# Kernel tuning notes

Hardware: AMD Instinct MI355X
Metric: run time of the kernel (lower is better)

## Reference

```python
import jax, jax.numpy as jnp
import numpy as np

N_NODES = 100000
N_EDGES = 3200000
N_FEAT = 512
HIDDEN = 16
N_CLASSES = 40


def gcn_conv(x, src, dst, W, b, num_nodes):
    # GCNConv with self-loops and symmetric normalization (default PyG settings).
    loop = jnp.arange(num_nodes)
    s = jnp.concatenate([src, loop])
    d = jnp.concatenate([dst, loop])
    deg = jax.ops.segment_sum(jnp.ones_like(s, dtype=x.dtype), d, num_segments=num_nodes)
    dinv = jnp.where(deg > 0, jax.lax.rsqrt(deg), 0.0)
    norm = dinv[s] * dinv[d]  # [E+N]
    h = x @ W  # [N, out]
    msg = h[s] * norm[:, None]  # gather + scale
    out = jax.ops.segment_sum(msg, d, num_segments=num_nodes)  # scatter-add
    return out + b


def setup_inputs() -> dict:
    key = jax.random.key(0)
    k1, k2, k3, k4 = jax.random.split(key, 4)
    x = jax.random.normal(k1, (N_NODES, N_FEAT), dtype=jnp.float32)
    edge_index = jax.random.randint(k2, (2, N_EDGES), 0, N_NODES, dtype=jnp.int64)
    W1 = jax.random.normal(k3, (N_FEAT, HIDDEN), dtype=jnp.float32) * 0.05
    b1 = jnp.zeros((HIDDEN,), dtype=jnp.float32)
    W2 = jax.random.normal(k4, (HIDDEN, N_CLASSES), dtype=jnp.float32) * 0.05
    b2 = jnp.zeros((N_CLASSES,), dtype=jnp.float32)
    return {"x": x, "edge_index": edge_index, "W1": W1, "b1": b1, "W2": W2, "b2": b2}


def reference(x, edge_index, W1, b1, W2, b2):
    num_nodes = x.shape[0]
    src, dst = edge_index[0], edge_index[1]
    h = gcn_conv(x, src, dst, W1, b1, num_nodes)
    h = jax.nn.relu(h)
    # dropout is identity in eval mode (training=False)
    out = gcn_conv(h, src, dst, W2, b2, num_nodes)
    return jax.nn.log_softmax(out, axis=1)
```

## Files before the change

### kernel.cpp

```cpp
#include <hip/hip_runtime.h>

#define N_NODES 100000
#define N_EDGES 3200000
#define N_FEAT 512
#define HIDDEN 16
#define N_CLASSES 40

#define SCAN_BLOCKS 98

#define CH    12800
#define NCH   8
#define NS    32
#define SLICE (N_EDGES / NS)
#define SL4   (SLICE / 4)

typedef int v4i __attribute__((ext_vector_type(4)));

__global__ __launch_bounds__(512) void k_p1(const int* __restrict__ dst,
                                            int* __restrict__ partS) {
    __shared__ int hist[CH];
    int tid = threadIdx.x;
    int s = blockIdx.x >> 3, j = blockIdx.x & 7;
    int base = j * CH;
    int lim = N_NODES - base; if (lim > CH) lim = CH;
    for (int i = tid; i < CH; i += 512) hist[i] = 0;
    __syncthreads();
    const v4i* dp = reinterpret_cast<const v4i*>(dst + s * SLICE);
    for (int i = tid; i < SL4; i += 512) {
        v4i d4 = __builtin_nontemporal_load(dp + i);
        unsigned a = (unsigned)(d4.x - base); if (a < (unsigned)lim) atomicAdd(&hist[a], 1);
        unsigned b = (unsigned)(d4.y - base); if (b < (unsigned)lim) atomicAdd(&hist[b], 1);
        unsigned c = (unsigned)(d4.z - base); if (c < (unsigned)lim) atomicAdd(&hist[c], 1);
        unsigned d = (unsigned)(d4.w - base); if (d < (unsigned)lim) atomicAdd(&hist[d], 1);
    }
    __syncthreads();
    for (int i = tid; i < lim; i += 512)
        partS[s * N_NODES + base + i] = hist[i];
}

__global__ __launch_bounds__(256) void k_colscan(int* __restrict__ partS,
                                                 int* __restrict__ deg,
                                                 float* __restrict__ dinv) {
    int n = blockIdx.x * 256 + threadIdx.x;
    if (n >= N_NODES) return;
    int run = 0;
    #pragma unroll
    for (int s = 0; s < NS; s++) {
        int idx = s * N_NODES + n;
        int v = partS[idx];
        partS[idx] = run;
        run += v;
    }
    deg[n] = run;
    dinv[n] = rsqrtf((float)(run + 1));
}


__global__ __launch_bounds__(1024) void k_scan_a(const int* __restrict__ cnt,
                                                 int* __restrict__ bsum) {
    int tid = threadIdx.x;
    int i = blockIdx.x * 1024 + tid;
    int v = (i < N_NODES) ? cnt[i] : 0;
    #pragma unroll
    for (int off = 32; off >= 1; off >>= 1) v += __shfl_xor(v, off, 64);
    __shared__ int ws[16];
    if ((tid & 63) == 0) ws[tid >> 6] = v;
    __syncthreads();
    if (tid == 0) {
        int s = 0;
        #pragma unroll
        for (int w = 0; w < 16; w++) s += ws[w];
        bsum[blockIdx.x] = s;
    }
}

__global__ __launch_bounds__(128) void k_scan_b(const int* __restrict__ bsum,
                                                int* __restrict__ boff) {
    int tid = threadIdx.x;
    int lane = tid & 63, wv = tid >> 6;
    int v = (tid < SCAN_BLOCKS) ? bsum[tid] : 0;
    int sc = v;
    #pragma unroll
    for (int off = 1; off < 64; off <<= 1) {
        int t = __shfl_up(sc, off, 64);
        if (lane >= off) sc += t;
    }
    __shared__ int wsum[2];
    if (lane == 63) wsum[wv] = sc;
    __syncthreads();
    int pre = (wv == 1) ? wsum[0] : 0;
    if (tid < SCAN_BLOCKS) boff[tid] = pre + sc - v;
}

__global__ __launch_bounds__(1024) void k_scan_c(const int* __restrict__ cnt,
                                                 const int* __restrict__ boff,
                                                 int* __restrict__ row_start) {
    int tid = threadIdx.x;
    int i = blockIdx.x * 1024 + tid;
    int lane = tid & 63, wv = tid >> 6;
    int v = (i < N_NODES) ? cnt[i] : 0;
    int sc = v;
    #pragma unroll
    for (int off = 1; off < 64; off <<= 1) {
        int t = __shfl_up(sc, off, 64);
        if (lane >= off) sc += t;
    }
    __shared__ int wsum[16];
    if (lane == 63) wsum[wv] = sc;
    __syncthreads();
    int pre = 0;
    #pragma unroll
    for (int w = 0; w < 16; w++) pre += (w < wv) ? wsum[w] : 0;
    int excl = boff[blockIdx.x] + pre + sc - v;
    if (i < N_NODES) row_start[i] = excl;
    if (i == N_NODES) row_start[N_NODES] = N_EDGES;
}

__global__ __launch_bounds__(512) void k_p2(const int* __restrict__ src,
                                            const int* __restrict__ dst,
                                            const int* __restrict__ partS,
                                            const int* __restrict__ row_start,
                                            const float* __restrict__ dinv,
                                            int2* __restrict__ edge_data) {
    __shared__ int cur[CH];
    int tid = threadIdx.x;
    int s = blockIdx.x >> 3, j = blockIdx.x & 7;
    int base = j * CH;
    int lim = N_NODES - base; if (lim > CH) lim = CH;
    for (int i = tid; i < lim; i += 512)
        cur[i] = row_start[base + i] + partS[s * N_NODES + base + i];
    __syncthreads();
    const v4i* dp = reinterpret_cast<const v4i*>(dst + s * SLICE);
    const v4i* sp = reinterpret_cast<const v4i*>(src + s * SLICE);
    for (int i = tid; i < SL4; i += 512) {
        v4i d4 = __builtin_nontemporal_load(dp + i);
        v4i s4 = __builtin_nontemporal_load(sp + i);
        {
            unsigned nl = (unsigned)(d4.x - base);
            if (nl < (unsigned)lim) {
                int slot = atomicAdd(&cur[nl], 1);
                edge_data[slot] = make_int2(s4.x, __float_as_int(dinv[s4.x] * dinv[d4.x]));
            }
        }
        {
            unsigned nl = (unsigned)(d4.y - base);
            if (nl < (unsigned)lim) {
                int slot = atomicAdd(&cur[nl], 1);
                edge_data[slot] = make_int2(s4.y, __float_as_int(dinv[s4.y] * dinv[d4.y]));
            }
        }
        {
            unsigned nl = (unsigned)(d4.z - base);
            if (nl < (unsigned)lim) {
                int slot = atomicAdd(&cur[nl], 1);
                edge_data[slot] = make_int2(s4.z, __float_as_int(dinv[s4.z] * dinv[d4.z]));
            }
        }
        {
            unsigned nl = (unsigned)(d4.w - base);
            if (nl < (unsigned)lim) {
                int slot = atomicAdd(&cur[nl], 1);
                edge_data[slot] = make_int2(s4.w, __float_as_int(dinv[s4.w] * dinv[d4.w]));
            }
        }
    }
}


#define KC 32
#define LDSW 36

__global__ __launch_bounds__(256) void k_gemm1(const float* __restrict__ x,
                                               const float* __restrict__ W1,
                                               float* __restrict__ h1) {
    __shared__ float xs[256 * LDSW];
    int tid = threadIdx.x;
    int row = blockIdx.x * 256 + tid;

    float acc[HIDDEN];
    #pragma unroll
    for (int j = 0; j < HIDDEN; j++) acc[j] = 0.f;

    int s_sub = tid >> 3;
    int s_k4  = tid & 7;

    for (int kc = 0; kc < N_FEAT; kc += KC) {
        __syncthreads();
        #pragma unroll
        for (int l = 0; l < 8; l++) {
            int srow = s_sub + l * 32;
            int grow = blockIdx.x * 256 + srow;
            int gr = grow < N_NODES ? grow : N_NODES - 1;
            float4 v = *reinterpret_cast<const float4*>(
                x + (size_t)gr * N_FEAT + kc + s_k4 * 4);
            *reinterpret_cast<float4*>(&xs[srow * LDSW + s_k4 * 4]) = v;
        }
        __syncthreads();

        const float* Wc = W1 + kc * HIDDEN;
        #pragma unroll
        for (int k4 = 0; k4 < 8; k4++) {
            float4 xv = *reinterpret_cast<const float4*>(&xs[tid * LDSW + k4 * 4]);
            const float* w0 = Wc + (k4 * 4 + 0) * HIDDEN;
            const float* w1 = Wc + (k4 * 4 + 1) * HIDDEN;
            const float* w2 = Wc + (k4 * 4 + 2) * HIDDEN;
            const float* w3 = Wc + (k4 * 4 + 3) * HIDDEN;
            #pragma unroll
            for (int j = 0; j < HIDDEN; j++) {
                acc[j] += xv.x * w0[j];
                acc[j] += xv.y * w1[j];
                acc[j] += xv.z * w2[j];
                acc[j] += xv.w * w3[j];
            }
        }
    }

    if (row < N_NODES) {
        float4* op = reinterpret_cast<float4*>(h1 + (size_t)row * HIDDEN);
        #pragma unroll
        for (int q = 0; q < 4; q++)
            op[q] = make_float4(acc[q*4+0], acc[q*4+1], acc[q*4+2], acc[q*4+3]);
    }
}


template <bool RELU>
__global__ __launch_bounds__(256) void k_agg16(const int2* __restrict__ edge_data,
                                               const int* __restrict__ row_start,
                                               const float* __restrict__ dinv,
                                               const float* __restrict__ h,
                                               const float* __restrict__ bias,
                                               float* __restrict__ out) {
    int g = threadIdx.x >> 4, j = threadIdx.x & 15;
    int node = blockIdx.x * 16 + g;
    if (node >= N_NODES) return;
    int beg = row_start[node], end = row_start[node + 1];
    float ds = dinv[node];
    float acc = h[(size_t)node * HIDDEN + j] * (ds * ds);
    int i = beg;
    for (; i + 3 < end; i += 4) {
        int2 e0 = edge_data[i + 0];
        int2 e1 = edge_data[i + 1];
        int2 e2 = edge_data[i + 2];
        int2 e3 = edge_data[i + 3];
        float v0 = h[(size_t)e0.x * HIDDEN + j];
        float v1 = h[(size_t)e1.x * HIDDEN + j];
        float v2 = h[(size_t)e2.x * HIDDEN + j];
        float v3 = h[(size_t)e3.x * HIDDEN + j];
        acc += v0 * __int_as_float(e0.y);
        acc += v1 * __int_as_float(e1.y);
        acc += v2 * __int_as_float(e2.y);
        acc += v3 * __int_as_float(e3.y);
    }
    for (; i < end; ++i) {
        int2 ed = edge_data[i];
        acc += h[(size_t)ed.x * HIDDEN + j] * __int_as_float(ed.y);
    }
    if (RELU) acc = fmaxf(acc + bias[j], 0.f);
    out[(size_t)node * HIDDEN + j] = acc;
}


__global__ __launch_bounds__(256) void k_out(const float* __restrict__ agg2,
                                             const float* __restrict__ W2,
                                             const float* __restrict__ b2,
                                             float* __restrict__ out) {
    int r = blockIdx.x * 256 + threadIdx.x;
    if (r >= N_NODES) return;
    float a[HIDDEN];
    const float4* ap = reinterpret_cast<const float4*>(agg2 + (size_t)r * HIDDEN);
    #pragma unroll
    for (int q = 0; q < 4; q++) {
        float4 v = ap[q];
        a[q * 4 + 0] = v.x; a[q * 4 + 1] = v.y;
        a[q * 4 + 2] = v.z; a[q * 4 + 3] = v.w;
    }
    float acc[N_CLASSES];
    #pragma unroll
    for (int jj = 0; jj < N_CLASSES; jj++) acc[jj] = b2[jj];
    #pragma unroll
    for (int kk = 0; kk < HIDDEN; kk++) {
        float av = a[kk];
        #pragma unroll
        for (int jj = 0; jj < N_CLASSES; jj++)
            acc[jj] += av * W2[kk * N_CLASSES + jj];
    }
    float m = -1e30f;
    #pragma unroll
    for (int jj = 0; jj < N_CLASSES; jj++) m = fmaxf(m, acc[jj]);
    float sum = 0.f;
    #pragma unroll
    for (int jj = 0; jj < N_CLASSES; jj++) sum += __expf(acc[jj] - m);
    float l = m + __logf(sum);
    float4* op = reinterpret_cast<float4*>(out + (size_t)r * N_CLASSES);
    #pragma unroll
    for (int q = 0; q < N_CLASSES / 4; q++) {
        op[q] = make_float4(acc[q*4+0] - l, acc[q*4+1] - l,
                            acc[q*4+2] - l, acc[q*4+3] - l);
    }
}


extern "C" void kernel_launch(void* const* d_in, const int* in_sizes, int n_in,
                              void* d_out, int out_size, void* d_ws, size_t ws_size,
                              hipStream_t stream) {
    const float* x  = (const float*)d_in[0];
    const int*   ei = (const int*)d_in[1];
    const float* W1 = (const float*)d_in[2];
    const float* b1 = (const float*)d_in[3];
    const float* W2 = (const float*)d_in[4];
    const float* b2 = (const float*)d_in[5];
    const int* src = ei;
    const int* dst = ei + N_EDGES;
    float* out = (float*)d_out;

    char* ws = (char*)d_ws;
    size_t off = 0;
    auto alloc = [&](size_t bytes) {
        size_t o = off; off = (off + bytes + 255) & ~(size_t)255; return o;
    };
    float* dinv      = (float*)(ws + alloc(sizeof(float) * N_NODES));
    int*   cnt       = (int*)  (ws + alloc(sizeof(int) * N_NODES));
    int*   row_start = (int*)  (ws + alloc(sizeof(int) * (N_NODES + 1)));
    int*   partS     = (int*)  (ws + alloc(sizeof(int) * (size_t)NS * N_NODES));
    int2*  edge_data = (int2*) (ws + alloc(sizeof(int2) * N_EDGES));
    float* h1        = (float*)(ws + alloc(sizeof(float) * N_NODES * HIDDEN));
    float* rbuf      = (float*)(ws + alloc(sizeof(float) * N_NODES * HIDDEN));
    float* agg2      = (float*)(ws + alloc(sizeof(float) * N_NODES * HIDDEN));
    int*   bsum      = (int*)  (ws + alloc(sizeof(int) * SCAN_BLOCKS));
    int*   boff      = (int*)  (ws + alloc(sizeof(int) * SCAN_BLOCKS));

    const int nodeBlocks  = (N_NODES + 255) / 256;
    const int aggBlocks   = (N_NODES + 15) / 16;
    const int csGrid      = NS * NCH;

    k_p1<<<csGrid, 512, 0, stream>>>(dst, partS);
    k_colscan<<<nodeBlocks, 256, 0, stream>>>(partS, cnt, dinv);
    k_scan_a<<<SCAN_BLOCKS, 1024, 0, stream>>>(cnt, bsum);
    k_scan_b<<<1, 128, 0, stream>>>(bsum, boff);
    k_scan_c<<<SCAN_BLOCKS, 1024, 0, stream>>>(cnt, boff, row_start);
    k_p2<<<csGrid, 512, 0, stream>>>(src, dst, partS, row_start, dinv, edge_data);

    k_gemm1<<<nodeBlocks, 256, 0, stream>>>(x, W1, h1);
    k_agg16<true><<<aggBlocks, 256, 0, stream>>>(edge_data, row_start, dinv, h1, b1, rbuf);
    k_agg16<false><<<aggBlocks, 256, 0, stream>>>(edge_data, row_start, dinv, rbuf, nullptr, agg2);
    k_out<<<nodeBlocks, 256, 0, stream>>>(agg2, W2, b2, out);
}
```

Measured before the change: 670.8 us.

## Replace single-pass CSR scatter with two-level bucket sort through staged buffer

The CSR build no longer has each of 256 blocks rescan every edge slice for an 8-way node partition. Edges are first bucketed by dst>>8 into 391 coarse chunks through a staged (src,dst) buffer. A per-chunk kernel then scatters them into final CSR slots, using LDS cursors and a cached dinv slice. This cuts the repeated global reads of dst/src and spreads the scattered writes, at the cost of extra kernels and an extra full pass over the edges. The staged buffer reuses the partS allocation, which is safe only because partS is consumed before the staging pass.

```diff
diff --git a/kernel.cpp b/kernel.cpp
--- a/kernel.cpp
+++ b/kernel.cpp
@@ -8,19 +8,26 @@
 
 #define SCAN_BLOCKS 98
 
-#define CH    12800
-#define NCH   8
+#define CH    16384
+#define NCH   7
 #define NS    32
 #define SLICE (N_EDGES / NS)
 #define SL4   (SLICE / 4)
 
+#define CH3   256
+#define NCHK  391
+#define NS2   256
+#define SLICE2 (N_EDGES / NS2)
+#define SL4_2  (SLICE2 / 4)
+
 typedef int v4i __attribute__((ext_vector_type(4)));
+typedef int v2i __attribute__((ext_vector_type(2)));
 
 __global__ __launch_bounds__(512) void k_p1(const int* __restrict__ dst,
                                             int* __restrict__ partS) {
     __shared__ int hist[CH];
     int tid = threadIdx.x;
-    int s = blockIdx.x >> 3, j = blockIdx.x & 7;
+    int s = blockIdx.x, j = blockIdx.y;
     int base = j * CH;
     int lim = N_NODES - base; if (lim > CH) lim = CH;
     for (int i = tid; i < CH; i += 512) hist[i] = 0;
@@ -38,19 +45,14 @@
         partS[s * N_NODES + base + i] = hist[i];
 }
 
-__global__ __launch_bounds__(256) void k_colscan(int* __restrict__ partS,
+__global__ __launch_bounds__(256) void k_colscan(const int* __restrict__ partS,
                                                  int* __restrict__ deg,
                                                  float* __restrict__ dinv) {
     int n = blockIdx.x * 256 + threadIdx.x;
     if (n >= N_NODES) return;
     int run = 0;
     #pragma unroll
-    for (int s = 0; s < NS; s++) {
-        int idx = s * N_NODES + n;
-        int v = partS[idx];
-        partS[idx] = run;
-        run += v;
-    }
+    for (int s = 0; s < NS; s++) run += partS[s * N_NODES + n];
     deg[n] = run;
     dinv[n] = rsqrtf((float)(run + 1));
 }
@@ -116,53 +118,110 @@
     if (i == N_NODES) row_start[N_NODES] = N_EDGES;
 }
 
-__global__ __launch_bounds__(512) void k_p2(const int* __restrict__ src,
-                                            const int* __restrict__ dst,
-                                            const int* __restrict__ partS,
+__global__ __launch_bounds__(512) void k_p1b(const int* __restrict__ dst,
+                                             int* __restrict__ cnt_sc) {
+    __shared__ int hist[NCHK];
+    int tid = threadIdx.x;
+    int s = blockIdx.x;
+    for (int i = tid; i < NCHK; i += 512) hist[i] = 0;
+    __syncthreads();
+    const v4i* dp = reinterpret_cast<const v4i*>(dst + s * SLICE2);
+    for (int i = tid; i < SL4_2; i += 512) {
+        v4i d4 = __builtin_nontemporal_load(dp + i);
+        atomicAdd(&hist[(unsigned)d4.x >> 8], 1);
+        atomicAdd(&hist[(unsigned)d4.y >> 8], 1);
+        atomicAdd(&hist[(unsigned)d4.z >> 8], 1);
+        atomicAdd(&hist[(unsigned)d4.w >> 8], 1);
+    }
+    __syncthreads();
+    for (int i = tid; i < NCHK; i += 512)
+        cnt_sc[s * NCHK + i] = hist[i];
+}
+
+__global__ __launch_bounds__(512) void k_scstage(const int* __restrict__ cnt_sc,
+                                                 int* __restrict__ sbase,
+                                                 int* __restrict__ cb) {
+    int tid = threadIdx.x;
+    int tot = 0;
+    if (tid < NCHK) {
+        int run = 0;
+        #pragma unroll 8
+        for (int s = 0; s < NS2; s++) {
+            int v = cnt_sc[s * NCHK + tid];
+            sbase[s * NCHK + tid] = run;
+            run += v;
+        }
+        tot = run;
+    }
+    int lane = tid & 63, wv = tid >> 6;
+    int sc = tot;
+    #pragma unroll
+    for (int off = 1; off < 64; off <<= 1) {
+        int t = __shfl_up(sc, off, 64);
+        if (lane >= off) sc += t;
+    }
+    __shared__ int wsum[8];
+    if (lane == 63) wsum[wv] = sc;
+    __syncthreads();
+    int pre = 0;
+    #pragma unroll
+    for (int w = 0; w < 8; w++) pre += (w < wv) ? wsum[w] : 0;
+    int excl = pre + sc - tot;
+    if (tid < NCHK) cb[tid] = excl;
+    if (tid == NCHK - 1) cb[NCHK] = excl + tot;
+}
+
+__global__ __launch_bounds__(512) void k_p2stage(const int* __restrict__ src,
+                                                 const int* __restrict__ dst,
+                                                 const int* __restrict__ sbase,
+                                                 const int* __restrict__ cb,
+                                                 int2* __restrict__ staged) {
+    __shared__ int curpos[NCHK];
+    int tid = threadIdx.x;
+    int s = blockIdx.x;
+    for (int c = tid; c < NCHK; c += 512)
+        curpos[c] = cb[c] + sbase[s * NCHK + c];
+    __syncthreads();
+    const v4i* dp = reinterpret_cast<const v4i*>(dst + s * SLICE2);
+    const v4i* sp = reinterpret_cast<const v4i*>(src + s * SLICE2);
+    for (int i = tid; i < SL4_2; i += 512) {
+        v4i d4 = __builtin_nontemporal_load(dp + i);
+        v4i s4 = __builtin_nontemporal_load(sp + i);
+        int p0 = atomicAdd(&curpos[(unsigned)d4.x >> 8], 1);
+        staged[p0] = make_int2(s4.x, d4.x);
+        int p1 = atomicAdd(&curpos[(unsigned)d4.y >> 8], 1);
+        staged[p1] = make_int2(s4.y, d4.y);
+        int p2 = atomicAdd(&curpos[(unsigned)d4.z >> 8], 1);
+        staged[p2] = make_int2(s4.z, d4.z);
+        int p3 = atomicAdd(&curpos[(unsigned)d4.w >> 8], 1);
+        staged[p3] = make_int2(s4.w, d4.w);
+    }
+}
+
+__global__ __launch_bounds__(512) void k_p3(const int2* __restrict__ staged,
+                                            const int* __restrict__ cb,
                                             const int* __restrict__ row_start,
                                             const float* __restrict__ dinv,
                                             int2* __restrict__ edge_data) {
-    __shared__ int cur[CH];
-    int tid = threadIdx.x;
-    int s = blockIdx.x >> 3, j = blockIdx.x & 7;
-    int base = j * CH;
-    int lim = N_NODES - base; if (lim > CH) lim = CH;
-    for (int i = tid; i < lim; i += 512)
-        cur[i] = row_start[base + i] + partS[s * N_NODES + base + i];
-    __syncthreads();
-    const v4i* dp = reinterpret_cast<const v4i*>(dst + s * SLICE);
-    const v4i* sp = reinterpret_cast<const v4i*>(src + s * SLICE);
-    for (int i = tid; i < SL4; i += 512) {
-        v4i d4 = __builtin_nontemporal_load(dp + i);
-        v4i s4 = __builtin_nontemporal_load(sp + i);
-        {
-            unsigned nl = (unsigned)(d4.x - base);
-            if (nl < (unsigned)lim) {
-                int slot = atomicAdd(&cur[nl], 1);
-                edge_data[slot] = make_int2(s4.x, __float_as_int(dinv[s4.x] * dinv[d4.x]));
-            }
-        }
-        {
-            unsigned nl = (unsigned)(d4.y - base);
-            if (nl < (unsigned)lim) {
-                int slot = atomicAdd(&cur[nl], 1);
-                edge_data[slot] = make_int2(s4.y, __float_as_int(dinv[s4.y] * dinv[d4.y]));
-            }
-        }
-        {
-            unsigned nl = (unsigned)(d4.z - base);
-            if (nl < (unsigned)lim) {
-                int slot = atomicAdd(&cur[nl], 1);
-                edge_data[slot] = make_int2(s4.z, __float_as_int(dinv[s4.z] * dinv[d4.z]));
-            }
-        }
-        {
-            unsigned nl = (unsigned)(d4.w - base);
-            if (nl < (unsigned)lim) {
-                int slot = atomicAdd(&cur[nl], 1);
-                edge_data[slot] = make_int2(s4.w, __float_as_int(dinv[s4.w] * dinv[d4.w]));
-            }
-        }
+    __shared__ int cur[CH3];
+    __shared__ float dv[CH3];
+    int tid = threadIdx.x;
+    int c = blockIdx.x;
+    int base = c << 8;
+    int lim = N_NODES - base; if (lim > CH3) lim = CH3;
+    if (tid < lim) {
+        cur[tid] = row_start[base + tid];
+        dv[tid]  = dinv[base + tid];
+    }
+    __syncthreads();
+    int beg = cb[c], end = cb[c + 1];
+    const v2i* stp = reinterpret_cast<const v2i*>(staged);
+    for (int i = beg + tid; i < end; i += 512) {
+        v2i e = __builtin_nontemporal_load(stp + i);
+        int nl = e.y - base;
+        float nrm = dinv[e.x] * dv[nl];
+        int slot = atomicAdd(&cur[nl], 1);
+        edge_data[slot] = make_int2(e.x, __float_as_int(nrm));
     }
 }
 
@@ -322,24 +381,30 @@
     float* dinv      = (float*)(ws + alloc(sizeof(float) * N_NODES));
     int*   cnt       = (int*)  (ws + alloc(sizeof(int) * N_NODES));
     int*   row_start = (int*)  (ws + alloc(sizeof(int) * (N_NODES + 1)));
+    int*   cnt_sc    = (int*)  (ws + alloc(sizeof(int) * NS2 * NCHK));
+    int*   sbase     = (int*)  (ws + alloc(sizeof(int) * NS2 * NCHK));
+    int*   cb        = (int*)  (ws + alloc(sizeof(int) * (NCHK + 1)));
     int*   partS     = (int*)  (ws + alloc(sizeof(int) * (size_t)NS * N_NODES));
-    int2*  edge_data = (int2*) (ws + alloc(sizeof(int2) * N_EDGES));
     float* h1        = (float*)(ws + alloc(sizeof(float) * N_NODES * HIDDEN));
     float* rbuf      = (float*)(ws + alloc(sizeof(float) * N_NODES * HIDDEN));
+    int2*  staged    = (int2*)partS;
+    int2*  edge_data = (int2*) (ws + alloc(sizeof(int2) * N_EDGES));
     float* agg2      = (float*)(ws + alloc(sizeof(float) * N_NODES * HIDDEN));
     int*   bsum      = (int*)  (ws + alloc(sizeof(int) * SCAN_BLOCKS));
     int*   boff      = (int*)  (ws + alloc(sizeof(int) * SCAN_BLOCKS));
 
     const int nodeBlocks  = (N_NODES + 255) / 256;
     const int aggBlocks   = (N_NODES + 15) / 16;
-    const int csGrid      = NS * NCH;
-
-    k_p1<<<csGrid, 512, 0, stream>>>(dst, partS);
+
+    k_p1<<<dim3(NS, NCH), 512, 0, stream>>>(dst, partS);
+    k_p1b<<<NS2, 512, 0, stream>>>(dst, cnt_sc);
     k_colscan<<<nodeBlocks, 256, 0, stream>>>(partS, cnt, dinv);
     k_scan_a<<<SCAN_BLOCKS, 1024, 0, stream>>>(cnt, bsum);
     k_scan_b<<<1, 128, 0, stream>>>(bsum, boff);
     k_scan_c<<<SCAN_BLOCKS, 1024, 0, stream>>>(cnt, boff, row_start);
-    k_p2<<<csGrid, 512, 0, stream>>>(src, dst, partS, row_start, dinv, edge_data);
+    k_scstage<<<1, 512, 0, stream>>>(cnt_sc, sbase, cb);
+    k_p2stage<<<NS2, 512, 0, stream>>>(src, dst, sbase, cb, staged);
+    k_p3<<<NCHK, 512, 0, stream>>>(staged, cb, row_start, dinv, edge_data);
 
     k_gemm1<<<nodeBlocks, 256, 0, stream>>>(x, W1, h1);
     k_agg16<true><<<aggBlocks, 256, 0, stream>>>(edge_data, row_start, dinv, h1, b1, rbuf);
```

New measurement: 581.9 us. 13.3% less time.
